# Kernel tuning notes

Hardware: AMD Instinct MI355X
Metric: run time of the kernel (lower is better)

The kernel has to match this reference:

```python
import jax, jax.numpy as jnp
from jax import lax
import numpy as np

BN_EPS = 1e-5


def _dwconv3x3(x, w):
    # x: [B,C,H,W], w: [C,1,3,3] depthwise (groups == C)
    return lax.conv_general_dilated(
        x, w, window_strides=(1, 1), padding='SAME',
        dimension_numbers=('NCHW', 'OIHW', 'NCHW'),
        feature_group_count=x.shape[1])


def _bn_eval(x, g, b, m, v):
    s = g * lax.rsqrt(v + BN_EPS)            # [C]
    return x * s[None, :, None, None] + (b - m * s)[None, :, None, None]


def _maxpool2(x):
    return lax.reduce_window(x, -jnp.inf, lax.max,
                             (1, 1, 2, 2), (1, 1, 2, 2), 'VALID')


def setup_inputs() -> dict:
    key = jax.random.key(0)
    ks = jax.random.split(key, 8)
    B, Cin, H, W = 32, 128, 64, 64
    Hd = 256               # hidden_size
    K, Ck = 32, 8          # num categories, hidden_size // K
    sc = 0.05
    return {
        'v4_features': jax.random.normal(ks[0], (B, Cin, H, W), jnp.float32),
        'w1_dw': jax.random.normal(ks[1], (Cin, 1, 3, 3), jnp.float32) * sc,
        'w1_pw': jax.random.normal(ks[2], (Hd, Cin), jnp.float32) * sc,
        'bn1_g': jnp.ones((Hd,), jnp.float32),
        'bn1_b': jnp.zeros((Hd,), jnp.float32),
        'bn1_m': jnp.zeros((Hd,), jnp.float32),
        'bn1_v': jnp.ones((Hd,), jnp.float32),
        'w2_dw': jax.random.normal(ks[3], (Hd, 1, 3, 3), jnp.float32) * sc,
        'w2_pw': jax.random.normal(ks[4], (Hd, Hd), jnp.float32) * sc,
        'bn2_g': jnp.ones((Hd,), jnp.float32),
        'bn2_b': jnp.zeros((Hd,), jnp.float32),
        'bn2_m': jnp.zeros((Hd,), jnp.float32),
        'bn2_v': jnp.ones((Hd,), jnp.float32),
        'cat_w': jax.random.normal(ks[5], (K, Ck, Hd), jnp.float32) * sc,
        'emb_w': jax.random.normal(ks[6], (128, Hd), jnp.float32) * sc,
        'emb_b': jnp.zeros((128,), jnp.float32),
    }


def reference(v4_features, w1_dw, w1_pw, bn1_g, bn1_b, bn1_m, bn1_v,
              w2_dw, w2_pw, bn2_g, bn2_b, bn2_m, bn2_v,
              cat_w, emb_w, emb_b):
    # Block 1: depthwise 3x3 -> pointwise 1x1 -> BN -> ReLU -> maxpool2
    x = _dwconv3x3(v4_features, w1_dw)
    x = jnp.einsum('bchw,oc->bohw', x, w1_pw)
    x = _maxpool2(jax.nn.relu(_bn_eval(x, bn1_g, bn1_b, bn1_m, bn1_v)))
    # Block 2
    x = _dwconv3x3(x, w2_dw)
    x = jnp.einsum('bchw,oc->bohw', x, w2_pw)
    x = _maxpool2(jax.nn.relu(_bn_eval(x, bn2_g, bn2_b, bn2_m, bn2_v)))
    # All 32 category 1x1 convs fused into one batched contraction.
    # cat_spikes: [B, K, Ck, H', W'] (non-SNN branch returns raw features)
    cat_spikes = jnp.einsum('bchw,koc->bkohw', x, cat_w)
    cat_pooled = cat_spikes.mean(axis=(-2, -1))         # [B, K, Ck]
    category_activations = cat_pooled.mean(axis=-1)     # [B, K]
    pooled = x.mean(axis=(-2, -1))                      # [B, Hd]
    object_embedding = pooled @ emb_w.T + emb_b         # [B, 128]
    return cat_spikes, category_activations, object_embedding, x
```

## Files before the change

### kernel.cpp

```cpp
#include <hip/hip_runtime.h>

#define BN_EPS 1e-5f

typedef float f32x4 __attribute__((ext_vector_type(4)));
typedef short short8 __attribute__((ext_vector_type(8)));
typedef unsigned short u16;

__device__ __forceinline__ u16 f2bf(float f) {
    unsigned u = __builtin_bit_cast(unsigned, f);
    unsigned r = (u + 0x7FFFu + ((u >> 16) & 1u)) >> 16;
    return (u16)r;
}
__device__ __forceinline__ float b2f(u16 h) {
    return __builtin_bit_cast(float, (unsigned)h << 16);
}

#define SWZ(row) ((((row) & 7) ^ (((row) >> 3) & 7)) << 4)

__global__ __launch_bounds__(256) void prep_bf16(
    const float* __restrict__ w1, const float* __restrict__ w2,
    const float* __restrict__ wc, u16* __restrict__ o1,
    u16* __restrict__ o2, u16* __restrict__ oc)
{
    const int idx = blockIdx.x * 256 + threadIdx.x;
    const float* src; u16* dst; int off;
    if (idx < 8192)       { src = w1; dst = o1; off = idx; }
    else if (idx < 24576) { src = w2; dst = o2; off = idx - 8192; }
    else                  { src = wc; dst = oc; off = idx - 24576; }
    const float4 v = *(const float4*)(src + 4 * (size_t)off);
    ushort4 h;
    h.x = f2bf(v.x); h.y = f2bf(v.y); h.z = f2bf(v.z); h.w = f2bf(v.w);
    *(ushort4*)(dst + 4 * (size_t)off) = h;
}

__global__ __launch_bounds__(256, 2) void b1_fused(
    const float* __restrict__ v4, const u16* __restrict__ wsW1,
    const float* __restrict__ w1dw,
    const float* __restrict__ bg, const float* __restrict__ bb,
    const float* __restrict__ bm, const float* __restrict__ bv,
    u16* __restrict__ t2b)
{
    __shared__ __align__(16) char smem[34816];
    float* sArr = (float*)(smem + 32768);
    float* tArr = (float*)(smem + 33792);

    const int bid = blockIdx.x;
    const int b   = bid >> 5;
    const int py  = bid & 31;
    const int t   = threadIdx.x;
    const int c    = t & 127;
    const int half = t >> 7;
    const int R    = 2 * py + half;

    {
        const float s = bg[t] * rsqrtf(bv[t] + BN_EPS);
        sArr[t] = s;
        tArr[t] = bb[t] - bm[t] * s;
    }

    float wt[9];
#pragma unroll
    for (int i = 0; i < 9; ++i) wt[i] = w1dw[c * 9 + i];

    {
        const float* vp = v4 + ((size_t)(b * 128 + c)) * 4096;
        float prevw[3] = {0.f, 0.f, 0.f};
#pragma unroll
        for (int ch = 0; ch < 4; ++ch) {
            const int x0 = ch * 16;
            float in[3][18];
#pragma unroll
            for (int j = 0; j < 3; ++j) {
                const int Rj = R - 1 + j;
                const bool ok = (Rj >= 0) && (Rj < 64);
                const float* rp = vp + Rj * 64 + x0;
                float4 q0, q1, q2, q3;
                if (ok) {
                    q0 = *(const float4*)(rp);
                    q1 = *(const float4*)(rp + 4);
                    q2 = *(const float4*)(rp + 8);
                    q3 = *(const float4*)(rp + 12);
                } else {
                    q0 = q1 = q2 = q3 = make_float4(0.f, 0.f, 0.f, 0.f);
                }
                in[j][0]  = prevw[j];
                in[j][1]  = q0.x; in[j][2]  = q0.y; in[j][3]  = q0.z; in[j][4]  = q0.w;
                in[j][5]  = q1.x; in[j][6]  = q1.y; in[j][7]  = q1.z; in[j][8]  = q1.w;
                in[j][9]  = q2.x; in[j][10] = q2.y; in[j][11] = q2.z; in[j][12] = q2.w;
                in[j][13] = q3.x; in[j][14] = q3.y; in[j][15] = q3.z; in[j][16] = q3.w;
                in[j][17] = (ok && ch < 3) ? rp[16] : 0.f;
                prevw[j] = q3.w;
            }
#pragma unroll
            for (int x = 0; x < 16; ++x) {
                float s = 0.f;
#pragma unroll
                for (int j = 0; j < 3; ++j)
                    s = fmaf(in[j][x], wt[3 * j],
                        fmaf(in[j][x + 1], wt[3 * j + 1],
                        fmaf(in[j][x + 2], wt[3 * j + 2], s)));
                const int p = half * 64 + x0 + x;
                *(u16*)(smem + ((p * 256 + 2 * c) ^ SWZ(p))) = f2bf(s);
            }
        }
    }
    __syncthreads();

    const int lane = t & 63, wid = t >> 6;
    const int lr = lane & 15, lg = lane >> 4;
    const int wo = wid * 64;

    f32x4 acc[4][8];
#pragma unroll
    for (int m = 0; m < 4; ++m)
#pragma unroll
        for (int n = 0; n < 8; ++n) acc[m][n] = (f32x4){0.f, 0.f, 0.f, 0.f};

    const u16* wbase = wsW1 + (size_t)(wo + lr) * 128 + lg * 8;
#pragma unroll
    for (int ks = 0; ks < 4; ++ks) {
        short8 af[4];
#pragma unroll
        for (int m = 0; m < 4; ++m)
            af[m] = *(const short8*)(wbase + m * 16 * 128 + ks * 32);
#pragma unroll
        for (int n = 0; n < 8; ++n) {
            const int prow = n * 16 + lr;
            const short8 bfv = *(const short8*)(smem +
                ((prow * 256 + ks * 64 + lg * 16) ^ SWZ(prow)));
#pragma unroll
            for (int m = 0; m < 4; ++m)
                acc[m][n] = __builtin_amdgcn_mfma_f32_16x16x32_bf16(af[m], bfv, acc[m][n], 0, 0, 0);
        }
    }

    u16* outb = t2b + ((size_t)(b * 256) * 32 + py) * 32;
#pragma unroll
    for (int m = 0; m < 4; ++m) {
#pragma unroll
        for (int j = 0; j < 4; ++j) {
            const int o = wo + m * 16 + 4 * lg + j;
            const float s = sArr[o], tt = tArr[o];
#pragma unroll
            for (int n = 0; n < 4; ++n) {
                const float a0 = fmaxf(fmaf(acc[m][n][j],     s, tt), 0.f);
                const float a1 = fmaxf(fmaf(acc[m][n + 4][j], s, tt), 0.f);
                const float vm = fmaxf(a0, a1);
                const float hm = fmaxf(vm, __shfl_xor(vm, 1));
                const unsigned p2 = (unsigned)f2bf(hm) |
                                    ((unsigned)f2bf(__shfl_xor(hm, 2)) << 16);
                const unsigned hi = __shfl_xor(p2, 4);
                if ((lr & 7) == 0) {
                    uint2 w2v; w2v.x = p2; w2v.y = hi;
                    *(uint2*)(outb + (size_t)o * 1024 + n * 8 + (lr >> 1)) = w2v;
                }
            }
        }
    }
}

template<int HW, int LOGW, int NPL, int IPP, int CMASK>
__global__ __launch_bounds__(256) void dw_shfl_bf(
    const u16* __restrict__ in, const float* __restrict__ wts,
    u16* __restrict__ out)
{
    const int t   = threadIdx.x;
    const int LPR = HW / 4;
    const int wq  = t & (LPR - 1);
    const int w0  = wq * 4;
    const int rin = t >> (LOGW - 2);

    for (int pl = 0; pl < NPL; ++pl) {
        const int plane = blockIdx.x * NPL + pl;
        const int c     = plane & CMASK;
        float wt[9];
#pragma unroll
        for (int i = 0; i < 9; ++i) wt[i] = wts[c * 9 + i];
        const u16* ip = in  + (size_t)plane * (HW * HW);
        u16*       op = out + (size_t)plane * (HW * HW);

#pragma unroll
        for (int it = 0; it < IPP; ++it) {
            const int h = it * (1024 / HW) + rin;
            const u16* rp = ip + h * HW + w0;
            float4 vc, vt, vb;
            {
                const ushort4 hcv = *(const ushort4*)rp;
                vc = make_float4(b2f(hcv.x), b2f(hcv.y), b2f(hcv.z), b2f(hcv.w));
            }
            if (h > 0) {
                const ushort4 htv = *(const ushort4*)(rp - HW);
                vt = make_float4(b2f(htv.x), b2f(htv.y), b2f(htv.z), b2f(htv.w));
            } else vt = make_float4(0.f, 0.f, 0.f, 0.f);
            if (h < HW - 1) {
                const ushort4 hbv = *(const ushort4*)(rp + HW);
                vb = make_float4(b2f(hbv.x), b2f(hbv.y), b2f(hbv.z), b2f(hbv.w));
            } else vb = make_float4(0.f, 0.f, 0.f, 0.f);

            float lc = __shfl_up(vc.w, 1),  rc = __shfl_down(vc.x, 1);
            float lt = __shfl_up(vt.w, 1),  rt = __shfl_down(vt.x, 1);
            float lb = __shfl_up(vb.w, 1),  rb = __shfl_down(vb.x, 1);
            if (wq == 0)       { lc = 0.f; lt = 0.f; lb = 0.f; }
            if (wq == LPR - 1) { rc = 0.f; rt = 0.f; rb = 0.f; }

            float o0 = 0.f, o1 = 0.f, o2 = 0.f, o3 = 0.f;
            o0 = fmaf(lt,   wt[0], fmaf(vt.x, wt[1], fmaf(vt.y, wt[2], o0)));
            o1 = fmaf(vt.x, wt[0], fmaf(vt.y, wt[1], fmaf(vt.z, wt[2], o1)));
            o2 = fmaf(vt.y, wt[0], fmaf(vt.z, wt[1], fmaf(vt.w, wt[2], o2)));
            o3 = fmaf(vt.z, wt[0], fmaf(vt.w, wt[1], fmaf(rt,   wt[2], o3)));
            o0 = fmaf(lc,   wt[3], fmaf(vc.x, wt[4], fmaf(vc.y, wt[5], o0)));
            o1 = fmaf(vc.x, wt[3], fmaf(vc.y, wt[4], fmaf(vc.z, wt[5], o1)));
            o2 = fmaf(vc.y, wt[3], fmaf(vc.z, wt[4], fmaf(vc.w, wt[5], o2)));
            o3 = fmaf(vc.z, wt[3], fmaf(vc.w, wt[4], fmaf(rc,   wt[5], o3)));
            o0 = fmaf(lb,   wt[6], fmaf(vb.x, wt[7], fmaf(vb.y, wt[8], o0)));
            o1 = fmaf(vb.x, wt[6], fmaf(vb.y, wt[7], fmaf(vb.z, wt[8], o1)));
            o2 = fmaf(vb.y, wt[6], fmaf(vb.z, wt[7], fmaf(vb.w, wt[8], o2)));
            o3 = fmaf(vb.z, wt[6], fmaf(vb.w, wt[7], fmaf(rb,   wt[8], o3)));

            ushort4 st;
            st.x = f2bf(o0); st.y = f2bf(o1); st.z = f2bf(o2); st.w = f2bf(o3);
            *(ushort4*)(op + h * HW + w0) = st;
        }
    }
}

__global__ __launch_bounds__(256) void pw2_mfma(
    const u16* __restrict__ t3b, const u16* __restrict__ wsW2,
    const float* __restrict__ bg, const float* __restrict__ bb,
    const float* __restrict__ bm, const float* __restrict__ bv,
    float* __restrict__ xout)
{
    __shared__ __align__(16) char smem[49664];
    float* sArr = (float*)(smem + 49152);
    float* tArr = (float*)(smem + 49408);
    float* Df   = (float*)smem;

    const int bid = blockIdx.x;
    const int o0  = ((bid >> 3) & 3) * 64;
    const int pxb = (bid >> 5) * 8 + (bid & 7);
    const int px  = pxb & 7;
    const int b   = pxb >> 3;
    const int p0  = px * 128;
    const int t   = threadIdx.x;

    const int lane = t & 63, wid = t >> 6;
    const int lr = lane & 15, lg = lane >> 4;
    const int wo = (wid >> 1) * 32;
    const int wp = (wid & 1) * 64;

    f32x4 acc[2][4];
#pragma unroll
    for (int m = 0; m < 2; ++m)
#pragma unroll
        for (int n = 0; n < 4; ++n) acc[m][n] = (f32x4){0.f, 0.f, 0.f, 0.f};

#pragma unroll
    for (int ko = 0; ko < 2; ++ko) {
        if (ko) __syncthreads();

#pragma unroll
        for (int i = 0; i < 4; ++i) {
            const int li = i * 256 + t;
            const int ol = li >> 4;
            const int f8 = li & 15;
            const short8 wv = *(const short8*)(wsW2 + (size_t)(o0 + ol) * 256 + ko * 128 + 8 * f8);
            *(short8*)(smem + ((ol * 256 + f8 * 16) ^ SWZ(ol))) = wv;
        }

        {
            const u16* xb = t3b + ((size_t)b * 256 + ko * 128) * 1024 + p0;
            const int pg = t & 15, cg = t >> 4;
            short8 vin[8];
#pragma unroll
            for (int j = 0; j < 8; ++j)
                vin[j] = *(const short8*)(xb + (size_t)(8 * cg + j) * 1024 + 8 * pg);
#pragma unroll
            for (int k = 0; k < 8; ++k) {
                short8 ov;
                ov[0] = vin[0][k]; ov[1] = vin[1][k]; ov[2] = vin[2][k]; ov[3] = vin[3][k];
                ov[4] = vin[4][k]; ov[5] = vin[5][k]; ov[6] = vin[6][k]; ov[7] = vin[7][k];
                const int row = 8 * pg + k;
                *(short8*)(smem + 16384 + ((row * 256 + cg * 16) ^ SWZ(row))) = ov;
            }
        }

        if (ko == 0 && t < 64) {
            const int o = o0 + t;
            const float s = bg[o] * rsqrtf(bv[o] + BN_EPS);
            sArr[t] = s;
            tArr[t] = bb[o] - bm[o] * s;
        }
        __syncthreads();

#pragma unroll
        for (int ks = 0; ks < 4; ++ks) {
            short8 af[2];
#pragma unroll
            for (int m = 0; m < 2; ++m) {
                const int rowm = wo + m * 16 + lr;
                af[m] = *(const short8*)(smem + ((rowm * 256 + ks * 64 + lg * 16) ^ SWZ(rowm)));
            }
#pragma unroll
            for (int n = 0; n < 4; ++n) {
                const int prow = wp + n * 16 + lr;
                const short8 bfv = *(const short8*)(smem + 16384 +
                    ((prow * 256 + ks * 64 + lg * 16) ^ SWZ(prow)));
                acc[0][n] = __builtin_amdgcn_mfma_f32_16x16x32_bf16(af[0], bfv, acc[0][n], 0, 0, 0);
                acc[1][n] = __builtin_amdgcn_mfma_f32_16x16x32_bf16(af[1], bfv, acc[1][n], 0, 0, 0);
            }
        }
    }
    __syncthreads();

    float sv[2][4], tv[2][4];
#pragma unroll
    for (int m = 0; m < 2; ++m)
#pragma unroll
        for (int j = 0; j < 4; ++j) {
            const int ol = wo + m * 16 + 4 * lg + j;
            sv[m][j] = sArr[ol];
            tv[m][j] = tArr[ol];
        }
#pragma unroll
    for (int m = 0; m < 2; ++m)
#pragma unroll
        for (int n = 0; n < 4; ++n)
#pragma unroll
            for (int j = 0; j < 4; ++j) {
                const int ol = wo + m * 16 + 4 * lg + j;
                const int pl = wp + n * 16 + lr;
                const float val = fmaf(acc[m][n][j], sv[m][j], tv[m][j]);
                Df[ol * 130 + pl] = fmaxf(val, 0.f);
            }
    __syncthreads();

#pragma unroll
    for (int i = 0; i < 8; ++i) {
        const int oi = i * 256 + t;
        const int o  = oi >> 5;
        const int q  = oi & 31;
        const int prl = q >> 4;
        const int pc  = q & 15;
        const float a0 = Df[o * 130 + prl * 64 + 2 * pc];
        const float a1 = Df[o * 130 + prl * 64 + 2 * pc + 1];
        const float b0 = Df[o * 130 + prl * 64 + 32 + 2 * pc];
        const float b1 = Df[o * 130 + prl * 64 + 32 + 2 * pc + 1];
        xout[(((size_t)(b * 256 + o0 + o)) * 16 + 2 * px + prl) * 16 + pc] =
            fmaxf(fmaxf(a0, a1), fmaxf(b0, b1));
    }
}

__global__ __launch_bounds__(256) void cat_mfma(
    const float* __restrict__ x, const u16* __restrict__ wsWc,
    float* __restrict__ spikes, float* __restrict__ cat_act)
{
    __shared__ __align__(16) char smem[36864];
    __shared__ float cs[4][32];
    __shared__ float msum[32];

    const int bid = blockIdx.x;
    const int b   = bid & 31;
    const int m0  = (bid >> 5) * 32;
    const int t   = threadIdx.x;

    const int lane = t & 63, wid = t >> 6;
    const int lr = lane & 15, lg = lane >> 4;
    const int wp = wid * 64;

    f32x4 acc[2][4];
#pragma unroll
    for (int m = 0; m < 2; ++m)
#pragma unroll
        for (int n = 0; n < 4; ++n) acc[m][n] = (f32x4){0.f, 0.f, 0.f, 0.f};

    const float* xb = x + (size_t)b * 65536;

#pragma unroll
    for (int ks = 0; ks < 4; ++ks) {
        if (ks) __syncthreads();

        if (t < 256) {
            const int ol = t >> 3;
            const int f8 = t & 7;
            const short8 wv = *(const short8*)(wsWc + (size_t)(m0 + ol) * 256 + ks * 64 + 8 * f8);
            *(short8*)(smem + ((ol * 128 + f8 * 16) ^ SWZ(ol))) = wv;
        }

#pragma unroll
        for (int i = 0; i < 4; ++i) {
            const int li = i * 256 + t;
            const int c4 = li >> 6;
            const int f4 = li & 63;
            float4 v0 = *(const float4*)(xb + (size_t)(ks * 64 + 4 * c4 + 0) * 256 + 4 * f4);
            float4 v1 = *(const float4*)(xb + (size_t)(ks * 64 + 4 * c4 + 1) * 256 + 4 * f4);
            float4 v2 = *(const float4*)(xb + (size_t)(ks * 64 + 4 * c4 + 2) * 256 + 4 * f4);
            float4 v3 = *(const float4*)(xb + (size_t)(ks * 64 + 4 * c4 + 3) * 256 + 4 * f4);
            ushort4 h0, h1, h2, h3;
            h0.x = f2bf(v0.x); h0.y = f2bf(v1.x); h0.z = f2bf(v2.x); h0.w = f2bf(v3.x);
            h1.x = f2bf(v0.y); h1.y = f2bf(v1.y); h1.z = f2bf(v2.y); h1.w = f2bf(v3.y);
            h2.x = f2bf(v0.z); h2.y = f2bf(v1.z); h2.z = f2bf(v2.z); h2.w = f2bf(v3.z);
            h3.x = f2bf(v0.w); h3.y = f2bf(v1.w); h3.z = f2bf(v2.w); h3.w = f2bf(v3.w);
            const int p_0 = 4 * f4;
            *(ushort4*)(smem + 4096 + (((p_0 + 0) * 128 + 8 * c4) ^ SWZ(p_0 + 0))) = h0;
            *(ushort4*)(smem + 4096 + (((p_0 + 1) * 128 + 8 * c4) ^ SWZ(p_0 + 1))) = h1;
            *(ushort4*)(smem + 4096 + (((p_0 + 2) * 128 + 8 * c4) ^ SWZ(p_0 + 2))) = h2;
            *(ushort4*)(smem + 4096 + (((p_0 + 3) * 128 + 8 * c4) ^ SWZ(p_0 + 3))) = h3;
        }
        __syncthreads();

#pragma unroll
        for (int kk = 0; kk < 2; ++kk) {
            short8 af[2];
#pragma unroll
            for (int m = 0; m < 2; ++m) {
                const int rowm = m * 16 + lr;
                af[m] = *(const short8*)(smem + ((rowm * 128 + kk * 64 + lg * 16) ^ SWZ(rowm)));
            }
#pragma unroll
            for (int n = 0; n < 4; ++n) {
                const int prow = wp + n * 16 + lr;
                const short8 bfv = *(const short8*)(smem + 4096 +
                    ((prow * 128 + kk * 64 + lg * 16) ^ SWZ(prow)));
                acc[0][n] = __builtin_amdgcn_mfma_f32_16x16x32_bf16(af[0], bfv, acc[0][n], 0, 0, 0);
                acc[1][n] = __builtin_amdgcn_mfma_f32_16x16x32_bf16(af[1], bfv, acc[1][n], 0, 0, 0);
            }
        }
    }

#pragma unroll
    for (int mi = 0; mi < 2; ++mi) {
#pragma unroll
        for (int j = 0; j < 4; ++j) {
            const int m = m0 + mi * 16 + 4 * lg + j;
#pragma unroll
            for (int n = 0; n < 4; ++n)
                spikes[((size_t)(b * 256 + m)) * 256 + wp + n * 16 + lr] = acc[mi][n][j];
            float s = acc[mi][0][j] + acc[mi][1][j] + acc[mi][2][j] + acc[mi][3][j];
            s += __shfl_xor(s, 1, 64);
            s += __shfl_xor(s, 2, 64);
            s += __shfl_xor(s, 4, 64);
            s += __shfl_xor(s, 8, 64);
            if (lr == 0) cs[wid][mi * 16 + 4 * lg + j] = s;
        }
    }
    __syncthreads();
    if (t < 32) msum[t] = cs[0][t] + cs[1][t] + cs[2][t] + cs[3][t];
    __syncthreads();
    if (t < 4) {
        float s = 0.f;
#pragma unroll
        for (int o = 0; o < 8; ++o) s += msum[t * 8 + o];
        cat_act[b * 32 + (m0 >> 3) + t] = s * (1.0f / 2048.0f);
    }
}

__global__ __launch_bounds__(256) void final_kernel(
    const float* __restrict__ x,
    const float* __restrict__ embw, const float* __restrict__ embb,
    float* __restrict__ emb)
{
    const int b = blockIdx.x;
    const int t = threadIdx.x;
    __shared__ __align__(16) float pooled[256];

    {
        const float4* src = (const float4*)(x + (size_t)b * 65536 + (size_t)t * 256);
        float s = 0.f;
#pragma unroll 8
        for (int i = 0; i < 64; ++i) {
            const float4 v = src[i];
            s += v.x + v.y + v.z + v.w;
        }
        pooled[t] = s * (1.0f / 256.0f);
    }
    __syncthreads();

    if (t < 128) {
        const float4* wr = (const float4*)(embw + (size_t)t * 256);
        float d = 0.f;
#pragma unroll 8
        for (int i = 0; i < 64; ++i) {
            const float4 wv = wr[i];
            const float4 pv = *(const float4*)&pooled[4 * i];
            d = fmaf(wv.x, pv.x, d);
            d = fmaf(wv.y, pv.y, d);
            d = fmaf(wv.z, pv.z, d);
            d = fmaf(wv.w, pv.w, d);
        }
        emb[b * 128 + t] = d + embb[t];
    }
}

extern "C" void kernel_launch(void* const* d_in, const int* in_sizes, int n_in,
                              void* d_out, int out_size, void* d_ws, size_t ws_size,
                              hipStream_t stream) {
    const float* v4   = (const float*)d_in[0];
    const float* w1dw = (const float*)d_in[1];
    const float* w1pw = (const float*)d_in[2];
    const float* bn1g = (const float*)d_in[3];
    const float* bn1b = (const float*)d_in[4];
    const float* bn1m = (const float*)d_in[5];
    const float* bn1v = (const float*)d_in[6];
    const float* w2dw = (const float*)d_in[7];
    const float* w2pw = (const float*)d_in[8];
    const float* bn2g = (const float*)d_in[9];
    const float* bn2b = (const float*)d_in[10];
    const float* bn2m = (const float*)d_in[11];
    const float* bn2v = (const float*)d_in[12];
    const float* catw = (const float*)d_in[13];
    const float* embw = (const float*)d_in[14];
    const float* embb = (const float*)d_in[15];

    float* out        = (float*)d_out;
    float* cat_spikes = out;
    float* cat_act    = out + 2097152;
    float* emb        = out + 2098176;
    float* xout       = out + 2102272;

    char* ws = (char*)d_ws;
    u16* wsW1 = (u16*)ws;
    u16* wsW2 = (u16*)(ws + 65536);
    u16* wsWc = (u16*)(ws + 196608);
    u16* t2b  = (u16*)(ws + 327680);
    u16* t3b  = (u16*)(ws + 327680 + 16777216);

    prep_bf16<<<160, 256, 0, stream>>>(w1pw, w2pw, catw, wsW1, wsW2, wsWc);
    b1_fused<<<1024, 256, 0, stream>>>(v4, wsW1, w1dw, bn1g, bn1b, bn1m, bn1v, t2b);
    dw_shfl_bf<32, 5, 4, 1, 255><<<2048, 256, 0, stream>>>(t2b, w2dw, t3b);
    pw2_mfma<<<1024, 256, 0, stream>>>(t3b, wsW2, bn2g, bn2b, bn2m, bn2v, xout);
    cat_mfma<<<256, 256, 0, stream>>>(xout, wsWc, cat_spikes, cat_act);
    final_kernel<<<32, 256, 0, stream>>>(xout, embw, embb, emb);
}
```

Measured before the change: 114.5 us.

## Split fused block-1 depthwise+pointwise kernel into separate dw and MFMA kernels

Replaces the fused block-1 kernel, which computed the 3x3 depthwise conv per thread into LDS and then ran the pointwise MFMA GEMM, with two kernels. A shuffle-based depthwise kernel reads fp32 input and writes a bf16 intermediate, and a new pointwise kernel loads that bf16 tile, transposes it into swizzled LDS and runs the same MFMA/BN/ReLU/maxpool epilogue. This aims to remove the poorly coalesced, register-heavy depthwise stage from the GEMM kernel. The cost is an extra 32 MB bf16 round trip through global memory and one more launch.

```diff
diff --git a/kernel.cpp b/kernel.cpp
--- a/kernel.cpp
+++ b/kernel.cpp
@@ -33,135 +33,9 @@
     *(ushort4*)(dst + 4 * (size_t)off) = h;
 }
 
-__global__ __launch_bounds__(256, 2) void b1_fused(
-    const float* __restrict__ v4, const u16* __restrict__ wsW1,
-    const float* __restrict__ w1dw,
-    const float* __restrict__ bg, const float* __restrict__ bb,
-    const float* __restrict__ bm, const float* __restrict__ bv,
-    u16* __restrict__ t2b)
-{
-    __shared__ __align__(16) char smem[34816];
-    float* sArr = (float*)(smem + 32768);
-    float* tArr = (float*)(smem + 33792);
-
-    const int bid = blockIdx.x;
-    const int b   = bid >> 5;
-    const int py  = bid & 31;
-    const int t   = threadIdx.x;
-    const int c    = t & 127;
-    const int half = t >> 7;
-    const int R    = 2 * py + half;
-
-    {
-        const float s = bg[t] * rsqrtf(bv[t] + BN_EPS);
-        sArr[t] = s;
-        tArr[t] = bb[t] - bm[t] * s;
-    }
-
-    float wt[9];
-#pragma unroll
-    for (int i = 0; i < 9; ++i) wt[i] = w1dw[c * 9 + i];
-
-    {
-        const float* vp = v4 + ((size_t)(b * 128 + c)) * 4096;
-        float prevw[3] = {0.f, 0.f, 0.f};
-#pragma unroll
-        for (int ch = 0; ch < 4; ++ch) {
-            const int x0 = ch * 16;
-            float in[3][18];
-#pragma unroll
-            for (int j = 0; j < 3; ++j) {
-                const int Rj = R - 1 + j;
-                const bool ok = (Rj >= 0) && (Rj < 64);
-                const float* rp = vp + Rj * 64 + x0;
-                float4 q0, q1, q2, q3;
-                if (ok) {
-                    q0 = *(const float4*)(rp);
-                    q1 = *(const float4*)(rp + 4);
-                    q2 = *(const float4*)(rp + 8);
-                    q3 = *(const float4*)(rp + 12);
-                } else {
-                    q0 = q1 = q2 = q3 = make_float4(0.f, 0.f, 0.f, 0.f);
-                }
-                in[j][0]  = prevw[j];
-                in[j][1]  = q0.x; in[j][2]  = q0.y; in[j][3]  = q0.z; in[j][4]  = q0.w;
-                in[j][5]  = q1.x; in[j][6]  = q1.y; in[j][7]  = q1.z; in[j][8]  = q1.w;
-                in[j][9]  = q2.x; in[j][10] = q2.y; in[j][11] = q2.z; in[j][12] = q2.w;
-                in[j][13] = q3.x; in[j][14] = q3.y; in[j][15] = q3.z; in[j][16] = q3.w;
-                in[j][17] = (ok && ch < 3) ? rp[16] : 0.f;
-                prevw[j] = q3.w;
-            }
-#pragma unroll
-            for (int x = 0; x < 16; ++x) {
-                float s = 0.f;
-#pragma unroll
-                for (int j = 0; j < 3; ++j)
-                    s = fmaf(in[j][x], wt[3 * j],
-                        fmaf(in[j][x + 1], wt[3 * j + 1],
-                        fmaf(in[j][x + 2], wt[3 * j + 2], s)));
-                const int p = half * 64 + x0 + x;
-                *(u16*)(smem + ((p * 256 + 2 * c) ^ SWZ(p))) = f2bf(s);
-            }
-        }
-    }
-    __syncthreads();
-
-    const int lane = t & 63, wid = t >> 6;
-    const int lr = lane & 15, lg = lane >> 4;
-    const int wo = wid * 64;
-
-    f32x4 acc[4][8];
-#pragma unroll
-    for (int m = 0; m < 4; ++m)
-#pragma unroll
-        for (int n = 0; n < 8; ++n) acc[m][n] = (f32x4){0.f, 0.f, 0.f, 0.f};
-
-    const u16* wbase = wsW1 + (size_t)(wo + lr) * 128 + lg * 8;
-#pragma unroll
-    for (int ks = 0; ks < 4; ++ks) {
-        short8 af[4];
-#pragma unroll
-        for (int m = 0; m < 4; ++m)
-            af[m] = *(const short8*)(wbase + m * 16 * 128 + ks * 32);
-#pragma unroll
-        for (int n = 0; n < 8; ++n) {
-            const int prow = n * 16 + lr;
-            const short8 bfv = *(const short8*)(smem +
-                ((prow * 256 + ks * 64 + lg * 16) ^ SWZ(prow)));
-#pragma unroll
-            for (int m = 0; m < 4; ++m)
-                acc[m][n] = __builtin_amdgcn_mfma_f32_16x16x32_bf16(af[m], bfv, acc[m][n], 0, 0, 0);
-        }
-    }
-
-    u16* outb = t2b + ((size_t)(b * 256) * 32 + py) * 32;
-#pragma unroll
-    for (int m = 0; m < 4; ++m) {
-#pragma unroll
-        for (int j = 0; j < 4; ++j) {
-            const int o = wo + m * 16 + 4 * lg + j;
-            const float s = sArr[o], tt = tArr[o];
-#pragma unroll
-            for (int n = 0; n < 4; ++n) {
-                const float a0 = fmaxf(fmaf(acc[m][n][j],     s, tt), 0.f);
-                const float a1 = fmaxf(fmaf(acc[m][n + 4][j], s, tt), 0.f);
-                const float vm = fmaxf(a0, a1);
-                const float hm = fmaxf(vm, __shfl_xor(vm, 1));
-                const unsigned p2 = (unsigned)f2bf(hm) |
-                                    ((unsigned)f2bf(__shfl_xor(hm, 2)) << 16);
-                const unsigned hi = __shfl_xor(p2, 4);
-                if ((lr & 7) == 0) {
-                    uint2 w2v; w2v.x = p2; w2v.y = hi;
-                    *(uint2*)(outb + (size_t)o * 1024 + n * 8 + (lr >> 1)) = w2v;
-                }
-            }
-        }
-    }
-}
-
 template<int HW, int LOGW, int NPL, int IPP, int CMASK>
-__global__ __launch_bounds__(256) void dw_shfl_bf(
-    const u16* __restrict__ in, const float* __restrict__ wts,
+__global__ __launch_bounds__(256) void dw_shfl(
+    const float* __restrict__ in, const float* __restrict__ wts,
     u16* __restrict__ out)
 {
     const int t   = threadIdx.x;
@@ -176,26 +50,17 @@
         float wt[9];
 #pragma unroll
         for (int i = 0; i < 9; ++i) wt[i] = wts[c * 9 + i];
-        const u16* ip = in  + (size_t)plane * (HW * HW);
-        u16*       op = out + (size_t)plane * (HW * HW);
+        const float* ip = in  + (size_t)plane * (HW * HW);
+        u16*         op = out + (size_t)plane * (HW * HW);
 
 #pragma unroll
         for (int it = 0; it < IPP; ++it) {
             const int h = it * (1024 / HW) + rin;
-            const u16* rp = ip + h * HW + w0;
-            float4 vc, vt, vb;
-            {
-                const ushort4 hcv = *(const ushort4*)rp;
-                vc = make_float4(b2f(hcv.x), b2f(hcv.y), b2f(hcv.z), b2f(hcv.w));
-            }
-            if (h > 0) {
-                const ushort4 htv = *(const ushort4*)(rp - HW);
-                vt = make_float4(b2f(htv.x), b2f(htv.y), b2f(htv.z), b2f(htv.w));
-            } else vt = make_float4(0.f, 0.f, 0.f, 0.f);
-            if (h < HW - 1) {
-                const ushort4 hbv = *(const ushort4*)(rp + HW);
-                vb = make_float4(b2f(hbv.x), b2f(hbv.y), b2f(hbv.z), b2f(hbv.w));
-            } else vb = make_float4(0.f, 0.f, 0.f, 0.f);
+            const float* rp = ip + h * HW + w0;
+            const float4 zero4 = make_float4(0.f, 0.f, 0.f, 0.f);
+            const float4 vc = *(const float4*)rp;
+            const float4 vt = (h > 0)      ? *(const float4*)(rp - HW) : zero4;
+            const float4 vb = (h < HW - 1) ? *(const float4*)(rp + HW) : zero4;
 
             float lc = __shfl_up(vc.w, 1),  rc = __shfl_down(vc.x, 1);
             float lt = __shfl_up(vt.w, 1),  rt = __shfl_down(vt.x, 1);
@@ -224,6 +89,164 @@
     }
 }
 
+__global__ __launch_bounds__(256, 2) void pw1_v2(
+    const u16* __restrict__ t1b, const u16* __restrict__ wsW1,
+    const float* __restrict__ bg, const float* __restrict__ bb,
+    const float* __restrict__ bm, const float* __restrict__ bv,
+    u16* __restrict__ t2b)
+{
+    __shared__ __align__(16) char smem[34816];
+    float* sArr = (float*)(smem + 32768);
+    float* tArr = (float*)(smem + 33792);
+
+    const int bid = blockIdx.x;
+    const int b   = bid >> 5;
+    const int py  = bid & 31;
+    const int p0  = py * 128;
+    const int t   = threadIdx.x;
+
+    {
+        const float s = bg[t] * rsqrtf(bv[t] + BN_EPS);
+        sArr[t] = s;
+        tArr[t] = bb[t] - bm[t] * s;
+    }
+
+    {
+        const u16* xb = t1b + ((size_t)b * 128) * 4096 + p0;
+        const int pg = t & 15, cg = t >> 4;
+        short8 vin[8];
+#pragma unroll
+        for (int j = 0; j < 8; ++j)
+            vin[j] = *(const short8*)(xb + (size_t)(8 * cg + j) * 4096 + 8 * pg);
+#pragma unroll
+        for (int k = 0; k < 8; ++k) {
+            short8 ov;
+            ov[0] = vin[0][k]; ov[1] = vin[1][k]; ov[2] = vin[2][k]; ov[3] = vin[3][k];
+            ov[4] = vin[4][k]; ov[5] = vin[5][k]; ov[6] = vin[6][k]; ov[7] = vin[7][k];
+            const int row = 8 * pg + k;
+            *(short8*)(smem + ((row * 256 + cg * 16) ^ SWZ(row))) = ov;
+        }
+    }
+    __syncthreads();
+
+    const int lane = t & 63, wid = t >> 6;
+    const int lr = lane & 15, lg = lane >> 4;
+    const int wo = wid * 64;
+
+    f32x4 acc[4][8];
+#pragma unroll
+    for (int m = 0; m < 4; ++m)
+#pragma unroll
+        for (int n = 0; n < 8; ++n) acc[m][n] = (f32x4){0.f, 0.f, 0.f, 0.f};
+
+    const u16* wbase = wsW1 + (size_t)(wo + lr) * 128 + lg * 8;
+#pragma unroll
+    for (int ks = 0; ks < 4; ++ks) {
+        short8 af[4];
+#pragma unroll
+        for (int m = 0; m < 4; ++m)
+            af[m] = *(const short8*)(wbase + m * 16 * 128 + ks * 32);
+#pragma unroll
+        for (int n = 0; n < 8; ++n) {
+            const int prow = n * 16 + lr;
+            const short8 bfv = *(const short8*)(smem +
+                ((prow * 256 + ks * 64 + lg * 16) ^ SWZ(prow)));
+#pragma unroll
+            for (int m = 0; m < 4; ++m)
+                acc[m][n] = __builtin_amdgcn_mfma_f32_16x16x32_bf16(af[m], bfv, acc[m][n], 0, 0, 0);
+        }
+    }
+
+    u16* outb = t2b + ((size_t)(b * 256) * 32 + py) * 32;
+#pragma unroll
+    for (int m = 0; m < 4; ++m) {
+#pragma unroll
+        for (int j = 0; j < 4; ++j) {
+            const int o = wo + m * 16 + 4 * lg + j;
+            const float s = sArr[o], tt = tArr[o];
+#pragma unroll
+            for (int n = 0; n < 4; ++n) {
+                const float a0 = fmaxf(fmaf(acc[m][n][j],     s, tt), 0.f);
+                const float a1 = fmaxf(fmaf(acc[m][n + 4][j], s, tt), 0.f);
+                const float vm = fmaxf(a0, a1);
+                const float hm = fmaxf(vm, __shfl_xor(vm, 1));
+                const unsigned p2 = (unsigned)f2bf(hm) |
+                                    ((unsigned)f2bf(__shfl_xor(hm, 2)) << 16);
+                const unsigned hi = __shfl_xor(p2, 4);
+                if ((lr & 7) == 0) {
+                    uint2 w2v; w2v.x = p2; w2v.y = hi;
+                    *(uint2*)(outb + (size_t)o * 1024 + n * 8 + (lr >> 1)) = w2v;
+                }
+            }
+        }
+    }
+}
+
+template<int HW, int LOGW, int NPL, int IPP, int CMASK>
+__global__ __launch_bounds__(256) void dw_shfl_bf(
+    const u16* __restrict__ in, const float* __restrict__ wts,
+    u16* __restrict__ out)
+{
+    const int t   = threadIdx.x;
+    const int LPR = HW / 4;
+    const int wq  = t & (LPR - 1);
+    const int w0  = wq * 4;
+    const int rin = t >> (LOGW - 2);
+
+    for (int pl = 0; pl < NPL; ++pl) {
+        const int plane = blockIdx.x * NPL + pl;
+        const int c     = plane & CMASK;
+        float wt[9];
+#pragma unroll
+        for (int i = 0; i < 9; ++i) wt[i] = wts[c * 9 + i];
+        const u16* ip = in  + (size_t)plane * (HW * HW);
+        u16*       op = out + (size_t)plane * (HW * HW);
+
+#pragma unroll
+        for (int it = 0; it < IPP; ++it) {
+            const int h = it * (1024 / HW) + rin;
+            const u16* rp = ip + h * HW + w0;
+            float4 vc, vt, vb;
+            {
+                const ushort4 hcv = *(const ushort4*)rp;
+                vc = make_float4(b2f(hcv.x), b2f(hcv.y), b2f(hcv.z), b2f(hcv.w));
+            }
+            if (h > 0) {
+                const ushort4 htv = *(const ushort4*)(rp - HW);
+                vt = make_float4(b2f(htv.x), b2f(htv.y), b2f(htv.z), b2f(htv.w));
+            } else vt = make_float4(0.f, 0.f, 0.f, 0.f);
+            if (h < HW - 1) {
+                const ushort4 hbv = *(const ushort4*)(rp + HW);
+                vb = make_float4(b2f(hbv.x), b2f(hbv.y), b2f(hbv.z), b2f(hbv.w));
+            } else vb = make_float4(0.f, 0.f, 0.f, 0.f);
+
+            float lc = __shfl_up(vc.w, 1),  rc = __shfl_down(vc.x, 1);
+            float lt = __shfl_up(vt.w, 1),  rt = __shfl_down(vt.x, 1);
+            float lb = __shfl_up(vb.w, 1),  rb = __shfl_down(vb.x, 1);
+            if (wq == 0)       { lc = 0.f; lt = 0.f; lb = 0.f; }
+            if (wq == LPR - 1) { rc = 0.f; rt = 0.f; rb = 0.f; }
+
+            float o0 = 0.f, o1 = 0.f, o2 = 0.f, o3 = 0.f;
+            o0 = fmaf(lt,   wt[0], fmaf(vt.x, wt[1], fmaf(vt.y, wt[2], o0)));
+            o1 = fmaf(vt.x, wt[0], fmaf(vt.y, wt[1], fmaf(vt.z, wt[2], o1)));
+            o2 = fmaf(vt.y, wt[0], fmaf(vt.z, wt[1], fmaf(vt.w, wt[2], o2)));
+            o3 = fmaf(vt.z, wt[0], fmaf(vt.w, wt[1], fmaf(rt,   wt[2], o3)));
+            o0 = fmaf(lc,   wt[3], fmaf(vc.x, wt[4], fmaf(vc.y, wt[5], o0)));
+            o1 = fmaf(vc.x, wt[3], fmaf(vc.y, wt[4], fmaf(vc.z, wt[5], o1)));
+            o2 = fmaf(vc.y, wt[3], fmaf(vc.z, wt[4], fmaf(vc.w, wt[5], o2)));
+            o3 = fmaf(vc.z, wt[3], fmaf(vc.w, wt[4], fmaf(rc,   wt[5], o3)));
+            o0 = fmaf(lb,   wt[6], fmaf(vb.x, wt[7], fmaf(vb.y, wt[8], o0)));
+            o1 = fmaf(vb.x, wt[6], fmaf(vb.y, wt[7], fmaf(vb.z, wt[8], o1)));
+            o2 = fmaf(vb.y, wt[6], fmaf(vb.z, wt[7], fmaf(vb.w, wt[8], o2)));
+            o3 = fmaf(vb.z, wt[6], fmaf(vb.w, wt[7], fmaf(rb,   wt[8], o3)));
+
+            ushort4 st;
+            st.x = f2bf(o0); st.y = f2bf(o1); st.z = f2bf(o2); st.w = f2bf(o3);
+            *(ushort4*)(op + h * HW + w0) = st;
+        }
+    }
+}
+
 __global__ __launch_bounds__(256) void pw2_mfma(
     const u16* __restrict__ t3b, const u16* __restrict__ wsW2,
     const float* __restrict__ bg, const float* __restrict__ bb,
@@ -379,7 +402,7 @@
     for (int ks = 0; ks < 4; ++ks) {
         if (ks) __syncthreads();
 
-        if (t < 256) {
+        {
             const int ol = t >> 3;
             const int f8 = t & 7;
             const short8 wv = *(const short8*)(wsWc + (size_t)(m0 + ol) * 256 + ks * 64 + 8 * f8);
@@ -521,11 +544,13 @@
     u16* wsW1 = (u16*)ws;
     u16* wsW2 = (u16*)(ws + 65536);
     u16* wsWc = (u16*)(ws + 196608);
-    u16* t2b  = (u16*)(ws + 327680);
-    u16* t3b  = (u16*)(ws + 327680 + 16777216);
+    u16* t1b  = (u16*)(ws + 327680);
+    u16* t2b  = (u16*)(ws + 327680 + 33554432);
+    u16* t3b  = (u16*)(ws + 327680 + 33554432 + 16777216);
 
     prep_bf16<<<160, 256, 0, stream>>>(w1pw, w2pw, catw, wsW1, wsW2, wsWc);
-    b1_fused<<<1024, 256, 0, stream>>>(v4, wsW1, w1dw, bn1g, bn1b, bn1m, bn1v, t2b);
+    dw_shfl<64, 6, 1, 4, 127><<<4096, 256, 0, stream>>>(v4, w1dw, t1b);
+    pw1_v2<<<1024, 256, 0, stream>>>(t1b, wsW1, bn1g, bn1b, bn1m, bn1v, t2b);
     dw_shfl_bf<32, 5, 4, 1, 255><<<2048, 256, 0, stream>>>(t2b, w2dw, t3b);
     pw2_mfma<<<1024, 256, 0, stream>>>(t3b, wsW2, bn2g, bn2b, bn2m, bn2v, xout);
     cat_mfma<<<256, 256, 0, stream>>>(xout, wsWc, cat_spikes, cat_act);
```

Measured after the change: 110.7 us. 1.03x faster.
